# Performance work log

Measured on AMD Instinct MI355X. Metric: run time of the kernel, lower is better.

Reference implementation:

```python
import jax, jax.numpy as jnp
import numpy as np

# Static problem sizes (uniform graphs for jit-friendliness)
B = 64          # number of hypergraphs in the batch
N_PER = 32      # shape-nodes per hypergraph (num_nodes_hgraph, uniform)
D_ID = 256      # shape_id_dim
D_MULT = 64     # shape_multiplicity_dim
LATENT = 512    # latent_dim
D_NODE = D_ID + D_MULT           # 320
FEAT = 3 * D_NODE + LATENT       # 1472, MLP input dim
HID = 2 * FEAT                   # 2944
NUM_ATOMS = 11                   # 1 + feature_sizes['num_atoms']
VOCAB_ID, VOCAB_MULT = 100, 20


def setup_inputs() -> dict:
    key = jax.random.key(0)
    ks = jax.random.split(key, 11)
    s1 = 1.0 / np.sqrt(FEAT)
    s2 = 1.0 / np.sqrt(HID)
    s3 = 1.0 / np.sqrt(FEAT)
    return {
        "shape_node_idx": jax.random.randint(ks[0], (B * N_PER,), 0, VOCAB_ID),
        "shape_node_mult": jax.random.randint(ks[1], (B * N_PER,), 0, VOCAB_MULT),
        "z_graph": jax.random.normal(ks[2], (B, LATENT), jnp.float32),
        "id_emb": jax.random.normal(ks[3], (VOCAB_ID, D_ID), jnp.float32) * 0.02,
        "mult_emb": jax.random.normal(ks[4], (VOCAB_MULT, D_MULT), jnp.float32) * 0.02,
        "W1": jax.random.normal(ks[5], (FEAT, HID), jnp.float32) * s1,
        "b1": jnp.zeros((HID,), jnp.float32),
        "W2": jax.random.normal(ks[6], (HID, FEAT), jnp.float32) * s2,
        "b2": jnp.zeros((FEAT,), jnp.float32),
        "W3": jax.random.normal(ks[7], (FEAT, NUM_ATOMS), jnp.float32) * s3,
        "b3": jnp.zeros((NUM_ATOMS,), jnp.float32),
    }


def reference(shape_node_idx, shape_node_mult, z_graph, id_emb, mult_emb,
              W1, b1, W2, b2, W3, b3):
    # Node features: concat of shape-id and multiplicity embeddings -> [B, n, d_node]
    x = jnp.concatenate([id_emb[shape_node_idx], mult_emb[shape_node_mult]], axis=-1)
    x = x.reshape(B, N_PER, D_NODE)

    # Per-graph segment aggregation (node_aggregation='mean') -> [B, d_node]
    agg = x.mean(axis=1)

    # All intra-graph node pairs (block-diagonal edge pattern), edge (i, j):
    # input = [x_i, x_j, z_graph, agg] broadcast to [B, n, n, FEAT]
    xi = jnp.broadcast_to(x[:, :, None, :], (B, N_PER, N_PER, D_NODE))
    xj = jnp.broadcast_to(x[:, None, :, :], (B, N_PER, N_PER, D_NODE))
    zg = jnp.broadcast_to(z_graph[:, None, None, :], (B, N_PER, N_PER, LATENT))
    ag = jnp.broadcast_to(agg[:, None, None, :], (B, N_PER, N_PER, D_NODE))
    feat = jnp.concatenate([xi, xj, zg, ag], axis=-1)  # [B, n, n, FEAT]

    # MLP [FEAT, 2*FEAT, FEAT, NUM_ATOMS] with ReLU activations
    h = jax.nn.relu(jnp.einsum('bijf,fh->bijh', feat, W1) + b1)
    h = jax.nn.relu(jnp.einsum('bijh,hf->bijf', h, W2) + b2)
    logits = jnp.einsum('bijf,fa->bija', h, W3) + b3  # [B, n, n, A]

    # _to_symmetric: average each edge value with its transpose
    logits = 0.5 * (logits + jnp.swapaxes(logits, 1, 2))

    # Flattened per-edge logits (matches sparse COO value order: row-major pairs)
    return logits.reshape(B * N_PER * N_PER, NUM_ATOMS)
```

## Files before the change

### kernel.cpp

```cpp
#include <hip/hip_runtime.h>
#include <stdint.h>

#define NBG   64
#define NPER  32
#define DNODE 320
#define FEAT  1472
#define HIDN  2944
#define FEATP 1536
#define NA    11
#define NROWS 2048
#define MEDGE 65536

typedef __attribute__((ext_vector_type(8))) short    bf16x8;
typedef __attribute__((ext_vector_type(4))) float    fv4;
typedef __attribute__((ext_vector_type(4))) unsigned uiv4;

__device__ __forceinline__ unsigned short f2bf(float f) {
  unsigned u = __builtin_bit_cast(unsigned, f);
  u += 0x7fffu + ((u >> 16) & 1u);
  return (unsigned short)(u >> 16);
}
__device__ __forceinline__ float bf2f(unsigned short h) {
  unsigned u = ((unsigned)h) << 16;
  return __builtin_bit_cast(float, u);
}
__device__ __forceinline__ unsigned cvt_pk_bf16(float lo, float hi) {
  unsigned r;
  asm("v_cvt_pk_bf16_f32 %0, %1, %2" : "=v"(r) : "v"(lo), "v"(hi));
  return r;
}
__device__ __forceinline__ void gload_lds16(const void* g, void* l) {
  __builtin_amdgcn_global_load_lds((const __attribute__((address_space(1))) void*)g,
                                   (__attribute__((address_space(3))) void*)l, 16, 0, 0);
}

__global__ void k_transpose_bf16(const float* __restrict__ src, unsigned short* __restrict__ dst,
                                 int K, int N, int Npad) {
  __shared__ float tile[64][65];
  int k0 = blockIdx.x * 64, n0 = blockIdx.y * 64;
  int r = threadIdx.x >> 2, cb = (threadIdx.x & 3) * 16;
  const float* srow = src + (size_t)(k0 + r) * N + n0 + cb;
#pragma unroll
  for (int c = 0; c < 16; ++c) {
    int n = n0 + cb + c;
    tile[r][cb + c] = (n < N) ? srow[c] : 0.f;
  }
  __syncthreads();
  unsigned short* drow = dst + (size_t)(n0 + r) * K + k0 + cb;
#pragma unroll
  for (int c = 0; c < 16; ++c) drow[c] = f2bf(tile[cb + c][r]);
}

__global__ void k_embed(const int* __restrict__ idx, const int* __restrict__ mlt,
                        const float* __restrict__ id_emb, const float* __restrict__ mult_emb,
                        unsigned short* __restrict__ xb) {
  int t = blockIdx.x, c = threadIdx.x;
  int iv = idx[t], mv = mlt[t];
  xb[t * DNODE + c] = f2bf(id_emb[iv * 256 + c]);
  if (c < 64) xb[t * DNODE + 256 + c] = f2bf(mult_emb[mv * 64 + c]);
}

__global__ void k_agg(const unsigned short* __restrict__ xb, float* __restrict__ agg) {
  int b = blockIdx.x;
  for (int d = threadIdx.x; d < DNODE; d += 256) {
    float s = 0.f;
    for (int i = 0; i < NPER; ++i) s += bf2f(xb[(b * NPER + i) * DNODE + d]);
    agg[b * DNODE + d] = s * (1.f / 32.f);
  }
}

__global__ void k_za(const float* __restrict__ z, const float* __restrict__ agg,
                     unsigned short* __restrict__ za) {
  int b = blockIdx.x;
  for (int c = threadIdx.x; c < 832; c += 256) {
    unsigned short v = 0;
    if (b < NBG) v = (c < 512) ? f2bf(z[b * 512 + c]) : f2bf(agg[b * DNODE + (c - 512)]);
    za[b * 832 + c] = v;
  }
}

__global__ void k_gemm1(const unsigned short* __restrict__ A, int sA, int Mrows,
                        const unsigned short* __restrict__ W1T, int kOff, int Ksteps,
                        float* __restrict__ C, const float* __restrict__ bias) {
  __shared__ alignas(16) unsigned short Als[128 * 32];
  __shared__ alignas(16) unsigned short Bls[128 * 32];
  int bx = blockIdx.x;
  int mt = bx / 23, nc = bx - mt * 23;
  int m0 = mt * 128, n0 = nc * 128;
  int tid = threadIdx.x, lane = tid & 63, w = tid >> 6;

  fv4 acc[4][4] = {};
  for (int kt = 0; kt < Ksteps; ++kt) {
    int k0 = kt * 32;
    __syncthreads();
#pragma unroll
    for (int q = 0; q < 2; ++q) {
      int seg = w * 2 + q;
      int row = seg * 16 + (lane >> 2);
      int col = (lane & 3) * 8;
      gload_lds16(A + (size_t)(m0 + row) * sA + k0 + col, &Als[seg * 512]);
      gload_lds16(W1T + (size_t)(n0 + row) * FEAT + kOff + k0 + col, &Bls[seg * 512]);
    }
    __syncthreads();
    bf16x8 aF[4], bF[4];
#pragma unroll
    for (int mf = 0; mf < 4; ++mf)
      aF[mf] = *(const bf16x8*)&Als[((w >> 1) * 64 + mf * 16 + (lane & 15)) * 32 + (lane >> 4) * 8];
#pragma unroll
    for (int nf = 0; nf < 4; ++nf)
      bF[nf] = *(const bf16x8*)&Bls[((w & 1) * 64 + nf * 16 + (lane & 15)) * 32 + (lane >> 4) * 8];
#pragma unroll
    for (int mf = 0; mf < 4; ++mf)
#pragma unroll
      for (int nf = 0; nf < 4; ++nf)
        acc[mf][nf] = __builtin_amdgcn_mfma_f32_16x16x32_bf16(aF[mf], bF[nf], acc[mf][nf], 0, 0, 0);
  }
  int mq = (w >> 1) * 64, nq = (w & 1) * 64;
#pragma unroll
  for (int mf = 0; mf < 4; ++mf)
#pragma unroll
    for (int nf = 0; nf < 4; ++nf) {
      int n = n0 + nq + nf * 16 + (lane & 15);
      float bv = bias ? bias[n] : 0.f;
#pragma unroll
      for (int r = 0; r < 4; ++r) {
        int m = m0 + mq + mf * 16 + (lane >> 4) * 4 + r;
        if (m < Mrows) C[(size_t)m * HIDN + n] = acc[mf][nf][r] + bv;
      }
    }
}

__global__ void k_pq(float* __restrict__ P1, const float* __restrict__ Q) {
  int r = blockIdx.x;
  const float* q = Q + (size_t)(r >> 5) * HIDN;
  float* p = P1 + (size_t)r * HIDN;
  for (int n = threadIdx.x; n < HIDN; n += 256) p[n] += q[n];
}

__global__ void k_zero(float* __restrict__ p, int n) {
  int i = blockIdx.x * 256 + threadIdx.x;
  if (i < n) p[i] = 0.f;
}

template <bool PARTIAL>
__global__ __launch_bounds__(256, 2)
void k_gemm2(const float* __restrict__ PQ1, const float* __restrict__ P2,
             const unsigned short* __restrict__ W2T,
             const float* __restrict__ b2, const float* __restrict__ W3,
             float* __restrict__ Lout) {
  __shared__ alignas(16) unsigned char LB[43008];
  int raw = blockIdx.x;
  int bx = (raw & 7) * 384 + (raw >> 3);
  int mt = bx / 6, nc2 = bx - mt * 6;
  int m0 = mt * 128, n0 = nc2 * 256;
  int tid = threadIdx.x, lane = tid & 63, w = tid >> 6;
  int bG = m0 >> 10;
  int i0 = (m0 >> 5) & 31;
  int ks = lane >> 4;
  int r  = lane & 15;

  const int swcolB = ((lane & 3) ^ ((lane >> 3) & 3)) * 8;
  const int swcolP = (((lane >> 1) & 3) ^ ((lane >> 3) & 3)) * 8 + (lane & 1) * 4;

  auto STAGEB = [&](int kt, int buf) {
#pragma unroll
    for (int q = 0; q < 4; ++q) {
      int seg = w * 4 + q;
      int row = seg * 16 + (lane >> 2);
      gload_lds16(W2T + (size_t)(n0 + row) * HIDN + kt * 32 + swcolB,
                  LB + buf * 16384 + seg * 1024);
    }
  };
  auto STAGESRC = [&](int kt, int buf) {
    gload_lds16(P2 + (size_t)(bG * NPER + 8 * w + (lane >> 3)) * HIDN + kt * 32 + swcolP,
                LB + 32768 + buf * 4096 + w * 1024);
    if (w == 0)
      gload_lds16(PQ1 + (size_t)(bG * NPER + i0 + (lane >> 3)) * HIDN + kt * 32 + (lane & 7) * 4,
                  LB + 40960 + buf * 1024);
  };

  fv4 acc[4][8] = {};

  STAGEB(0, 0);
  STAGESRC(0, 0);
  __syncthreads();

  for (int kt = 0; kt < 92; ++kt) {
    int cur = kt & 1, nxt = cur ^ 1;
    if (kt < 91) { STAGEB(kt + 1, nxt); STAGESRC(kt + 1, nxt); }

    const unsigned char* Bb = LB + cur * 16384;
    const unsigned char* Pb = LB + 32768 + cur * 4096;
    const unsigned char* Qb = LB + 40960 + cur * 1024;

    int il0 = (w >> 1) * 2;
    int psw = (ks ^ (r & 3)) * 32;
    fv4 q0[2], q1[2], p0[2], p1[2];
#pragma unroll
    for (int h = 0; h < 2; ++h) {
      q0[h] = *(const fv4*)(Qb + il0 * 128 + ks * 32 + h * 16);
      q1[h] = *(const fv4*)(Qb + (il0 + 1) * 128 + ks * 32 + h * 16);
      p0[h] = *(const fv4*)(Pb + r * 128 + psw + h * 16);
      p1[h] = *(const fv4*)(Pb + (16 + r) * 128 + psw + h * 16);
    }
    bf16x8 bF[8];
#pragma unroll
    for (int nf = 0; nf < 8; ++nf) {
      int brow = (w & 1) * 128 + nf * 16 + r;
      int slot = ks ^ ((brow >> 1) & 3);
      bF[nf] = *(const bf16x8*)(Bb + brow * 64 + slot * 16);
    }

    bf16x8 aF[4];
#pragma unroll
    for (int mf = 0; mf < 4; ++mf) {
      fv4 s0 = (mf & 2 ? q1[0] : q0[0]) + (mf & 1 ? p1[0] : p0[0]);
      fv4 s1 = (mf & 2 ? q1[1] : q0[1]) + (mf & 1 ? p1[1] : p0[1]);
      uiv4 u;
      u[0] = cvt_pk_bf16(fmaxf(s0[0], 0.f), fmaxf(s0[1], 0.f));
      u[1] = cvt_pk_bf16(fmaxf(s0[2], 0.f), fmaxf(s0[3], 0.f));
      u[2] = cvt_pk_bf16(fmaxf(s1[0], 0.f), fmaxf(s1[1], 0.f));
      u[3] = cvt_pk_bf16(fmaxf(s1[2], 0.f), fmaxf(s1[3], 0.f));
      aF[mf] = __builtin_bit_cast(bf16x8, u);
    }

#pragma unroll
    for (int nf = 0; nf < 8; ++nf)
#pragma unroll
      for (int mf = 0; mf < 4; ++mf)
        acc[mf][nf] = __builtin_amdgcn_mfma_f32_16x16x32_bf16(aF[mf], bF[nf], acc[mf][nf], 0, 0, 0);
    __syncthreads();
  }

  float* red = (float*)LB;
  int nq = (w & 1) * 128;
#pragma unroll
  for (int mf = 0; mf < 4; ++mf) {
    float s[4][NA];
#pragma unroll
    for (int rr = 0; rr < 4; ++rr)
#pragma unroll
      for (int a = 0; a < NA; ++a) s[rr][a] = 0.f;
#pragma unroll
    for (int nf = 0; nf < 8; ++nf) {
      int n = n0 + nq + nf * 16 + r;
      if (n < FEAT) {
        float bv = b2[n];
        float w3r[NA];
#pragma unroll
        for (int a = 0; a < NA; ++a) w3r[a] = W3[n * NA + a];
#pragma unroll
        for (int rr = 0; rr < 4; ++rr) {
          float h = fmaxf(acc[mf][nf][rr] + bv, 0.f);
#pragma unroll
          for (int a = 0; a < NA; ++a) s[rr][a] += h * w3r[a];
        }
      }
    }
#pragma unroll
    for (int off = 1; off < 16; off <<= 1)
#pragma unroll
      for (int rr = 0; rr < 4; ++rr)
#pragma unroll
        for (int a = 0; a < NA; ++a) s[rr][a] += __shfl_xor(s[rr][a], off, 64);
    int a = r;
    if (a < NA) {
#pragma unroll
      for (int rr = 0; rr < 4; ++rr)
        red[w * 704 + (mf * 16 + ks * 4 + rr) * NA + a] = s[rr][a];
    }
  }
  __syncthreads();
  for (int e = tid; e < 128 * NA; e += 256) {
    int row = e / NA, a = e - row * NA;
    int wr = row >> 6, rr = row & 63;
    float v = red[(wr * 2 + 0) * 704 + rr * NA + a] + red[(wr * 2 + 1) * 704 + rr * NA + a];
    if (PARTIAL)
      Lout[(size_t)nc2 * (MEDGE * NA) + (size_t)(m0 + row) * NA + a] = v;
    else
      atomicAdd(&Lout[(size_t)(m0 + row) * NA + a], v);
  }
}

template <int NS>
__global__ void k_sym(const float* __restrict__ LRp, const float* __restrict__ b3,
                      float* __restrict__ out) {
  int e = blockIdx.x * 256 + threadIdx.x;
  if (e >= MEDGE * NA) return;
  int m = e / NA, a = e - m * NA;
  int msw = (m & ~1023) | ((m & 31) << 5) | ((m >> 5) & 31);
  float s = 0.f;
#pragma unroll
  for (int t = 0; t < NS; ++t)
    s += LRp[(size_t)t * (MEDGE * NA) + e] + LRp[(size_t)t * (MEDGE * NA) + (size_t)msw * NA + a];
  out[e] = 0.5f * s + b3[a];
}

extern "C" void kernel_launch(void* const* d_in, const int* in_sizes, int n_in,
                              void* d_out, int out_size, void* d_ws, size_t ws_size,
                              hipStream_t stream) {
  const int*   idx      = (const int*)d_in[0];
  const int*   mlt      = (const int*)d_in[1];
  const float* z        = (const float*)d_in[2];
  const float* id_emb   = (const float*)d_in[3];
  const float* mult_emb = (const float*)d_in[4];
  const float* W1       = (const float*)d_in[5];
  const float* b1       = (const float*)d_in[6];
  const float* W2       = (const float*)d_in[7];
  const float* b2       = (const float*)d_in[8];
  const float* W3       = (const float*)d_in[9];
  const float* b3       = (const float*)d_in[10];
  float* out = (float*)d_out;

  uint8_t* ws = (uint8_t*)d_ws;
  size_t o = 0;
  auto alloc = [&](size_t bytes) { size_t r = o; o += (bytes + 255) & ~(size_t)255; return r; };
  size_t oW1T = alloc((size_t)HIDN * FEAT * 2);
  size_t oW2T = alloc((size_t)FEATP * HIDN * 2);
  size_t oXB  = alloc((size_t)NROWS * DNODE * 2);
  size_t oZA  = alloc((size_t)128 * 832 * 2);
  size_t oAG  = alloc((size_t)NBG * DNODE * 4);
  size_t oP1  = alloc((size_t)NROWS * HIDN * 4);
  size_t oP2  = alloc((size_t)NROWS * HIDN * 4);
  size_t oQ   = alloc((size_t)NBG * HIDN * 4);
  size_t oLRp = alloc((size_t)6 * MEDGE * NA * 4);
  size_t needPartial = o;
  size_t needAtomic  = oLRp + (((size_t)MEDGE * NA * 4 + 255) & ~(size_t)255);
  if (ws_size < needAtomic) return;
  bool partial = (ws_size >= needPartial);

  unsigned short* W1T = (unsigned short*)(ws + oW1T);
  unsigned short* W2T = (unsigned short*)(ws + oW2T);
  unsigned short* xb  = (unsigned short*)(ws + oXB);
  unsigned short* za  = (unsigned short*)(ws + oZA);
  float* agg = (float*)(ws + oAG);
  float* P1  = (float*)(ws + oP1);
  float* P2  = (float*)(ws + oP2);
  float* Qm  = (float*)(ws + oQ);
  float* LRp = (float*)(ws + oLRp);

  k_transpose_bf16<<<dim3(FEAT / 64, HIDN / 64), 256, 0, stream>>>(W1, W1T, FEAT, HIDN, HIDN);
  k_transpose_bf16<<<dim3(HIDN / 64, FEATP / 64), 256, 0, stream>>>(W2, W2T, HIDN, FEAT, FEATP);
  k_embed<<<NROWS, 256, 0, stream>>>(idx, mlt, id_emb, mult_emb, xb);
  k_agg<<<NBG, 256, 0, stream>>>(xb, agg);
  k_za<<<128, 256, 0, stream>>>(z, agg, za);
  k_gemm1<<<16 * 23, 256, 0, stream>>>(xb, DNODE, NROWS, W1T, 0, 10, P1, nullptr);
  k_gemm1<<<16 * 23, 256, 0, stream>>>(xb, DNODE, NROWS, W1T, 320, 10, P2, nullptr);
  k_gemm1<<<1 * 23, 256, 0, stream>>>(za, 832, NBG, W1T, 640, 26, Qm, b1);
  k_pq<<<NROWS, 256, 0, stream>>>(P1, Qm);

  if (partial) {
    k_gemm2<true><<<512 * 6, 256, 0, stream>>>(P1, P2, W2T, b2, W3, LRp);
    k_sym<6><<<(MEDGE * NA + 255) / 256, 256, 0, stream>>>(LRp, b3, out);
  } else {
    k_zero<<<(MEDGE * NA + 255) / 256, 256, 0, stream>>>(LRp, MEDGE * NA);
    k_gemm2<false><<<512 * 6, 256, 0, stream>>>(P1, P2, W2T, b2, W3, LRp);
    k_sym<1><<<(MEDGE * NA + 255) / 256, 256, 0, stream>>>(LRp, b3, out);
  }
}
```

Before: 1.154 ms.

## Use packed add/relu in gemm2 A-build and always reduce via atomics

The per-iteration A-fragment construction in the second GEMM now uses packed f32 adds and a packed i16 max on bf16 pairs for ReLU, replacing scalar fmaxf calls, to cut VALU work in the hot loop. The partial-sum path with six separate output slabs is removed. Partial results are always accumulated with atomicAdd into a single zeroed buffer, and the symmetrize kernel reads only one slab. This trades fewer memory writes and reads in the final stage for atomic contention and an extra zeroing kernel.

Result: no change. 1.144 ms (-0.8%).

```diff
diff --git a/kernel.cpp b/kernel.cpp
--- a/kernel.cpp
+++ b/kernel.cpp
@@ -13,6 +13,7 @@
 
 typedef __attribute__((ext_vector_type(8))) short    bf16x8;
 typedef __attribute__((ext_vector_type(4))) float    fv4;
+typedef __attribute__((ext_vector_type(2))) float    fv2;
 typedef __attribute__((ext_vector_type(4))) unsigned uiv4;
 
 __device__ __forceinline__ unsigned short f2bf(float f) {
@@ -29,6 +30,18 @@
   asm("v_cvt_pk_bf16_f32 %0, %1, %2" : "=v"(r) : "v"(lo), "v"(hi));
   return r;
 }
+__device__ __forceinline__ fv2 pk_add(fv2 a, fv2 b) {
+  fv2 d;
+  asm("v_pk_add_f32 %0, %1, %2" : "=v"(d) : "v"(a), "v"(b));
+  return d;
+}
+__device__ __forceinline__ unsigned pk_relu2(unsigned x, unsigned z) {
+  unsigned r;
+  asm("v_pk_max_i16 %0, %1, %2" : "=v"(r) : "v"(x), "v"(z));
+  return r;
+}
+__device__ __forceinline__ fv2 lo2(fv4 v) { return __builtin_shufflevector(v, v, 0, 1); }
+__device__ __forceinline__ fv2 hi2(fv4 v) { return __builtin_shufflevector(v, v, 2, 3); }
 __device__ __forceinline__ void gload_lds16(const void* g, void* l) {
   __builtin_amdgcn_global_load_lds((const __attribute__((address_space(1))) void*)g,
                                    (__attribute__((address_space(3))) void*)l, 16, 0, 0);
@@ -142,7 +155,6 @@
   if (i < n) p[i] = 0.f;
 }
 
-template <bool PARTIAL>
 __global__ __launch_bounds__(256, 2)
 void k_gemm2(const float* __restrict__ PQ1, const float* __restrict__ P2,
              const unsigned short* __restrict__ W2T,
@@ -180,11 +192,14 @@
   };
 
   fv4 acc[4][8] = {};
+  unsigned z0 = 0;
+  asm volatile("" : "+v"(z0));
 
   STAGEB(0, 0);
   STAGESRC(0, 0);
   __syncthreads();
 
+  int il0 = (w >> 1) * 2;
   for (int kt = 0; kt < 92; ++kt) {
     int cur = kt & 1, nxt = cur ^ 1;
     if (kt < 91) { STAGEB(kt + 1, nxt); STAGESRC(kt + 1, nxt); }
@@ -193,7 +208,6 @@
     const unsigned char* Pb = LB + 32768 + cur * 4096;
     const unsigned char* Qb = LB + 40960 + cur * 1024;
 
-    int il0 = (w >> 1) * 2;
     int psw = (ks ^ (r & 3)) * 32;
     fv4 q0[2], q1[2], p0[2], p1[2];
 #pragma unroll
@@ -214,13 +228,19 @@
     bf16x8 aF[4];
 #pragma unroll
     for (int mf = 0; mf < 4; ++mf) {
-      fv4 s0 = (mf & 2 ? q1[0] : q0[0]) + (mf & 1 ? p1[0] : p0[0]);
-      fv4 s1 = (mf & 2 ? q1[1] : q0[1]) + (mf & 1 ? p1[1] : p0[1]);
+      fv4 qa0 = (mf & 2) ? q1[0] : q0[0];
+      fv4 qa1 = (mf & 2) ? q1[1] : q0[1];
+      fv4 pa0 = (mf & 1) ? p1[0] : p0[0];
+      fv4 pa1 = (mf & 1) ? p1[1] : p0[1];
+      fv2 s00 = pk_add(lo2(qa0), lo2(pa0));
+      fv2 s01 = pk_add(hi2(qa0), hi2(pa0));
+      fv2 s10 = pk_add(lo2(qa1), lo2(pa1));
+      fv2 s11 = pk_add(hi2(qa1), hi2(pa1));
       uiv4 u;
-      u[0] = cvt_pk_bf16(fmaxf(s0[0], 0.f), fmaxf(s0[1], 0.f));
-      u[1] = cvt_pk_bf16(fmaxf(s0[2], 0.f), fmaxf(s0[3], 0.f));
-      u[2] = cvt_pk_bf16(fmaxf(s1[0], 0.f), fmaxf(s1[1], 0.f));
-      u[3] = cvt_pk_bf16(fmaxf(s1[2], 0.f), fmaxf(s1[3], 0.f));
+      u[0] = pk_relu2(cvt_pk_bf16(s00[0], s00[1]), z0);
+      u[1] = pk_relu2(cvt_pk_bf16(s01[0], s01[1]), z0);
+      u[2] = pk_relu2(cvt_pk_bf16(s10[0], s10[1]), z0);
+      u[3] = pk_relu2(cvt_pk_bf16(s11[0], s11[1]), z0);
       aF[mf] = __builtin_bit_cast(bf16x8, u);
     }
 
@@ -275,25 +295,17 @@
     int row = e / NA, a = e - row * NA;
     int wr = row >> 6, rr = row & 63;
     float v = red[(wr * 2 + 0) * 704 + rr * NA + a] + red[(wr * 2 + 1) * 704 + rr * NA + a];
-    if (PARTIAL)
-      Lout[(size_t)nc2 * (MEDGE * NA) + (size_t)(m0 + row) * NA + a] = v;
-    else
-      atomicAdd(&Lout[(size_t)(m0 + row) * NA + a], v);
-  }
-}
-
-template <int NS>
-__global__ void k_sym(const float* __restrict__ LRp, const float* __restrict__ b3,
+    atomicAdd(&Lout[(size_t)(m0 + row) * NA + a], v);
+  }
+}
+
+__global__ void k_sym(const float* __restrict__ Lraw, const float* __restrict__ b3,
                       float* __restrict__ out) {
   int e = blockIdx.x * 256 + threadIdx.x;
   if (e >= MEDGE * NA) return;
   int m = e / NA, a = e - m * NA;
   int msw = (m & ~1023) | ((m & 31) << 5) | ((m >> 5) & 31);
-  float s = 0.f;
-#pragma unroll
-  for (int t = 0; t < NS; ++t)
-    s += LRp[(size_t)t * (MEDGE * NA) + e] + LRp[(size_t)t * (MEDGE * NA) + (size_t)msw * NA + a];
-  out[e] = 0.5f * s + b3[a];
+  out[e] = 0.5f * (Lraw[e] + Lraw[(size_t)msw * NA + a]) + b3[a];
 }
 
 extern "C" void kernel_launch(void* const* d_in, const int* in_sizes, int n_in,
@@ -323,11 +335,8 @@
   size_t oP1  = alloc((size_t)NROWS * HIDN * 4);
   size_t oP2  = alloc((size_t)NROWS * HIDN * 4);
   size_t oQ   = alloc((size_t)NBG * HIDN * 4);
-  size_t oLRp = alloc((size_t)6 * MEDGE * NA * 4);
-  size_t needPartial = o;
-  size_t needAtomic  = oLRp + (((size_t)MEDGE * NA * 4 + 255) & ~(size_t)255);
-  if (ws_size < needAtomic) return;
-  bool partial = (ws_size >= needPartial);
+  size_t oLR  = alloc((size_t)MEDGE * NA * 4);
+  if (ws_size < o) return;
 
   unsigned short* W1T = (unsigned short*)(ws + oW1T);
   unsigned short* W2T = (unsigned short*)(ws + oW2T);
@@ -337,7 +346,7 @@
   float* P1  = (float*)(ws + oP1);
   float* P2  = (float*)(ws + oP2);
   float* Qm  = (float*)(ws + oQ);
-  float* LRp = (float*)(ws + oLRp);
+  float* LR  = (float*)(ws + oLR);
 
   k_transpose_bf16<<<dim3(FEAT / 64, HIDN / 64), 256, 0, stream>>>(W1, W1T, FEAT, HIDN, HIDN);
   k_transpose_bf16<<<dim3(HIDN / 64, FEATP / 64), 256, 0, stream>>>(W2, W2T, HIDN, FEAT, FEATP);
@@ -348,13 +357,7 @@
   k_gemm1<<<16 * 23, 256, 0, stream>>>(xb, DNODE, NROWS, W1T, 320, 10, P2, nullptr);
   k_gemm1<<<1 * 23, 256, 0, stream>>>(za, 832, NBG, W1T, 640, 26, Qm, b1);
   k_pq<<<NROWS, 256, 0, stream>>>(P1, Qm);
-
-  if (partial) {
-    k_gemm2<true><<<512 * 6, 256, 0, stream>>>(P1, P2, W2T, b2, W3, LRp);
-    k_sym<6><<<(MEDGE * NA + 255) / 256, 256, 0, stream>>>(LRp, b3, out);
-  } else {
-    k_zero<<<(MEDGE * NA + 255) / 256, 256, 0, stream>>>(LRp, MEDGE * NA);
-    k_gemm2<false><<<512 * 6, 256, 0, stream>>>(P1, P2, W2T, b2, W3, LRp);
-    k_sym<1><<<(MEDGE * NA + 255) / 256, 256, 0, stream>>>(LRp, b3, out);
-  }
-}
+  k_zero<<<(MEDGE * NA + 255) / 256, 256, 0, stream>>>(LR, MEDGE * NA);
+  k_gemm2<<<512 * 6, 256, 0, stream>>>(P1, P2, W2T, b2, W3, LR);
+  k_sym<<<(MEDGE * NA + 255) / 256, 256, 0, stream>>>(LR, b3, out);
+}
```
